# Kernel tuning notes

Hardware: AMD Instinct MI355X
Metric: run time of the kernel (lower is better)

Reference implementation:

```python
import jax, jax.numpy as jnp
import numpy as np

RANK = 8
ALPHA = 16.0
SCALING = ALPHA / RANK


def setup_inputs() -> dict:
    key = jax.random.key(0)
    ks = jax.random.split(key, 13)
    T, B, D = 8, 1024, 1024
    H1, H2, H3 = 2048, 2048, 1024
    r = RANK
    def n(k, shape, scale):
        return jax.random.normal(k, shape, dtype=jnp.float32) * scale
    return {
        "x": n(ks[0], (T, B, D), 1.0),
        "k0": n(ks[1], (D, H1), D ** -0.5),
        "b0": n(ks[2], (H1,), 0.02),
        "d0": n(ks[3], (D, r, T), D ** -0.5),
        "u0": n(ks[4], (r, H1, T), 0.02),  # zeros-init in original; random for nontrivial test
        "k1": n(ks[5], (H1, H2), H1 ** -0.5),
        "b1": n(ks[6], (H2,), 0.02),
        "d1": n(ks[7], (H1, r, T), H1 ** -0.5),
        "u1": n(ks[8], (r, H2, T), 0.02),
        "k2": n(ks[9], (H2, H3), H2 ** -0.5),
        "b2": n(ks[10], (H3,), 0.02),
        "d2": n(ks[11], (H2, r, T), H2 ** -0.5),
        "u2": n(ks[12], (r, H3, T), 0.02),
    }


def _lora_dense(h, k, b, d, u):
    # frozen base matmul: [t,b,i] @ [i,f] -> [t,b,f]
    base = jnp.einsum('tbi,if->tbf', h, k) + b
    # per-task low-rank adapter: down [i,r,t], up [r,f,t]
    delta = jnp.einsum('tbi,irt,rft->tbf', h, d, u) * SCALING
    return base + delta


def reference(x, k0, b0, d0, u0, k1, b1, d1, u1, k2, b2, d2, u2):
    h = jax.nn.relu(_lora_dense(x, k0, b0, d0, u0))
    h = jax.nn.relu(_lora_dense(h, k1, b1, d1, u1))
    h = _lora_dense(h, k2, b2, d2, u2)  # no activation on final layer
    return h
```

## Files before the change

kernel.cpp:

```cpp
#include <hip/hip_runtime.h>

typedef unsigned short u16;
typedef __attribute__((ext_vector_type(8))) __bf16 bf16x8;
typedef __attribute__((ext_vector_type(8))) unsigned short u16x8;
typedef __attribute__((ext_vector_type(4))) float f32x4;

__device__ __forceinline__ float bf2f(u16 h) {
    return __uint_as_float(((unsigned int)h) << 16);
}
__device__ __forceinline__ u16 f2bf(float f) {
    unsigned int u = __float_as_uint(f);
    u += 0x7fffu + ((u >> 16) & 1u);
    return (u16)(u >> 16);
}
__device__ __forceinline__ bf16x8 zero_bf16x8() {
    union { unsigned int u[4]; bf16x8 v; } z;
    z.u[0] = z.u[1] = z.u[2] = z.u[3] = 0u;
    return z.v;
}
__device__ __forceinline__ void gload_lds16(const void* g, void* l) {
    __builtin_amdgcn_global_load_lds(
        (const __attribute__((address_space(1))) unsigned int*)g,
        (__attribute__((address_space(3))) unsigned int*)l, 16, 0, 0);
}
__device__ __forceinline__ void store_out(u16* p, float v)  { *p = f2bf(v); }
__device__ __forceinline__ void store_out(float* p, float v){ *p = v; }


__device__ __forceinline__ void do_cvt(
    const float* __restrict__ in, u16* __restrict__ out, int blk)
{
    int i = (blk * 256 + (int)threadIdx.x) * 8;
    float4 a = *(const float4*)(in + i);
    float4 b = *(const float4*)(in + i + 4);
    u16x8 o;
    o[0] = f2bf(a.x); o[1] = f2bf(a.y); o[2] = f2bf(a.z); o[3] = f2bf(a.w);
    o[4] = f2bf(b.x); o[5] = f2bf(b.y); o[6] = f2bf(b.z); o[7] = f2bf(b.w);
    *(u16x8*)(out + i) = o;
}

__device__ __forceinline__ void do_transpose(
    const float* __restrict__ in, u16* __restrict__ out, int K, int F, int t)
{
    __shared__ u16 tt[32][33];
    int fb = t % (F >> 5), kb = t / (F >> 5);
    int f0 = fb << 5, k0 = kb << 5;
    int lx = threadIdx.x & 31;
    int ly = threadIdx.x >> 5;
#pragma unroll
    for (int i = 0; i < 4; ++i) {
        int k = ly + i * 8;
        tt[k][lx] = f2bf(in[(size_t)(k0 + k) * F + f0 + lx]);
    }
    __syncthreads();
#pragma unroll
    for (int i = 0; i < 4; ++i) {
        int fy = ly + i * 8;
        out[(size_t)(f0 + fy) * K + k0 + lx] = tt[lx][fy];
    }
}

__device__ __forceinline__ void do_prep_d(
    const float* __restrict__ d, u16* __restrict__ o, int K, int blk)
{
    int i = blk * 256 + (int)threadIdx.x;
    int r = i & 7;
    int k = (i >> 3) % K;
    int t = i / (K * 8);
    o[i] = f2bf(d[((size_t)k * 8 + r) * 8 + t]);
}

__device__ __forceinline__ void do_prep_u(
    const float* __restrict__ u, u16* __restrict__ o, int F, int blk)
{
    int i = blk * 256 + (int)threadIdx.x;
    int r = i & 7;
    int f = (i >> 3) % F;
    int t = i / (F * 8);
    o[i] = f2bf(u[((size_t)r * F + f) * 8 + t] * 2.0f);
}

__global__ __launch_bounds__(256) void prep_all(
    const float* x, const float* k0, const float* k1, const float* k2,
    const float* d0, const float* d1, const float* d2,
    const float* u0, const float* u1, const float* u2,
    u16* xb, u16* k0T, u16* k1T, u16* k2T,
    u16* dS0, u16* dS1, u16* dS2, u16* uS0, u16* uS1, u16* uS2)
{
    int b = blockIdx.x;
    if      (b < 4096)  do_cvt(x, xb, b);
    else if (b < 6144)  do_transpose(k0, k0T, 1024, 2048, b - 4096);
    else if (b < 10240) do_transpose(k1, k1T, 2048, 2048, b - 6144);
    else if (b < 12288) do_transpose(k2, k2T, 2048, 1024, b - 10240);
    else if (b < 12544) do_prep_d(d0, dS0, 1024, b - 12288);
    else if (b < 13056) do_prep_d(d1, dS1, 2048, b - 12544);
    else if (b < 13568) do_prep_d(d2, dS2, 2048, b - 13056);
    else if (b < 14080) do_prep_u(u0, uS0, 2048, b - 13568);
    else if (b < 14592) do_prep_u(u1, uS1, 2048, b - 14080);
    else                do_prep_u(u2, uS2, 1024, b - 14592);
}

__global__ __launch_bounds__(256) void lora_down(
    const u16* __restrict__ H, const u16* __restrict__ dS,
    u16* __restrict__ Aout, int K)
{
    int gt   = blockIdx.x * 256 + threadIdx.x;
    int row  = gt >> 3;
    int oct  = gt & 7;
    int task = row >> 10;
    const u16* hrow = H  + (size_t)row * K;
    const u16* dt   = dS + (size_t)task * K * 8;
    float acc[8];
#pragma unroll
    for (int r = 0; r < 8; ++r) acc[r] = 0.f;
    int kpt  = K >> 3;
    int kbeg = oct * kpt;
    for (int kk = kbeg; kk < kbeg + kpt; kk += 8) {
        u16x8 h8 = *(const u16x8*)(hrow + kk);
#pragma unroll
        for (int j = 0; j < 8; ++j) {
            float hv = bf2f(h8[j]);
            u16x8 dv = *(const u16x8*)(dt + (size_t)(kk + j) * 8);
#pragma unroll
            for (int r = 0; r < 8; ++r)
                acc[r] += hv * bf2f(dv[r]);
        }
    }
#pragma unroll
    for (int r = 0; r < 8; ++r) {
        acc[r] += __shfl_xor(acc[r], 1);
        acc[r] += __shfl_xor(acc[r], 2);
        acc[r] += __shfl_xor(acc[r], 4);
    }
    if (oct == 0) {
        u16x8 o;
#pragma unroll
        for (int r = 0; r < 8; ++r) o[r] = f2bf(acc[r]);
        *(u16x8*)(Aout + (size_t)row * 8) = o;
    }
}


#define WVMC do { if constexpr (BN == 256) { \
                    asm volatile("s_waitcnt vmcnt(4)" ::: "memory"); \
                  } else { \
                    asm volatile("s_waitcnt vmcnt(3)" ::: "memory"); } } while (0)
#define WVM0  asm volatile("s_waitcnt vmcnt(0)" ::: "memory")
#define PHASE_END do { __builtin_amdgcn_sched_barrier(0); \
                       __builtin_amdgcn_s_barrier(); } while (0)

#define DS_A(c, mh) do { \
    _Pragma("unroll") for (int mm = 0; mm < 4; ++mm) \
    _Pragma("unroll") for (int ks = 0; ks < 2; ++ks) \
        aF[mm][ks] = *(const bf16x8*)((const char*)&sA[c][0] + \
                       arowb + ((mh)*4+mm)*4096 + (ks ? cb1 : cb0)); } while (0)

#define DS_B(c, nh, bset) do { \
    _Pragma("unroll") for (int nn = 0; nn < NBH; ++nn) \
    _Pragma("unroll") for (int ks = 0; ks < 2; ++ks) \
        bset[nn][ks] = *(const bf16x8*)((const char*)&sB[c][0] + \
                       browb + ((nh)*NBH+nn)*8192 + (ks ? cb1 : cb0)); } while (0)

#define MFMAQ(mh, nh, bset) do { \
    _Pragma("unroll") for (int ks = 0; ks < 2; ++ks) \
    _Pragma("unroll") for (int mm = 0; mm < 4; ++mm) \
    _Pragma("unroll") for (int nn = 0; nn < NBH; ++nn) \
        acc[(mh)*4+mm][(nh)*NBH+nn] = __builtin_amdgcn_mfma_f32_16x16x32_bf16( \
            aF[mm][ks], bset[nn][ks], acc[(mh)*4+mm][(nh)*NBH+nn], 0, 0, 0); } while (0)

#define STAGE_A(c, h, kt) do { \
    _Pragma("unroll") for (int s = 0; s < 2; ++s) \
        gload_lds16((const char*)A + (size_t)(unsigned)(aBase + \
                      ((h)*128 + s*64)*(K*2) + (kt)*128), \
                    (char*)&sA[c][0] + (h)*16384 + s*8192 + tdst); } while (0)

#define STAGE_B(c, h, kt) do { \
    _Pragma("unroll") for (int s = 0; s < SBL; ++s) \
        gload_lds16((const char*)BT + (size_t)(unsigned)(bBase + \
                      ((h)*BNH + s*64)*(K*2) + (kt)*128), \
                    (char*)&sB[c][0] + (h)*(BNH*128) + s*8192 + tdst); } while (0)

template<int RELU, int BN, typename OUT_T>
__global__ __launch_bounds__(512, 2) void gemm_lora8(
    const u16* __restrict__ A, const u16* __restrict__ BT,
    const u16* __restrict__ ALR, const u16* __restrict__ US,
    const float* __restrict__ bias, OUT_T* __restrict__ C,
    int N, int K)
{
    constexpr int SBL = BN / 128;
    constexpr int NBH = BN / 128;
    constexpr int NBN = BN / 64;
    constexpr int BNH = BN / 2;

    __shared__ __align__(16) u16 sA[2][256 * 64];
    __shared__ __align__(16) u16 sB[2][BN * 64];

    const int tid  = threadIdx.x;
    const int lane = tid & 63;
    const int wave = tid >> 6;
    const int wr   = wave >> 2;
    const int wc   = wave & 3;
    const int l15  = lane & 15;
    const int lg   = lane >> 4;

    const int nwg = gridDim.x;
    const int orig = blockIdx.x;
    const int q = nwg >> 3, r = nwg & 7;
    const int x = orig & 7, o = orig >> 3;
    const int wg = (x < r ? x * (q + 1) : r * (q + 1) + (x - r) * q) + o;
    const int nbn  = N / BN;
    const int bm   = wg / nbn;
    const int bn   = wg % nbn;
    const int brow = bm << 8;
    const int bcol = bn * BN;
    const int task = brow >> 10;

    const int trow = tid >> 3;
    const int tkc  = (tid & 7) ^ (trow & 7);
    const int tdst = tid * 16;
    const int aBase = (brow + trow) * (K * 2) + tkc * 16;
    const int bBase = (bcol + trow) * (K * 2) + tkc * 16;

    const int rp    = l15 & 7;
    const int cb0   = ((lg ^ (rp & 3)) << 4) | ((rp & 4) << 4);
    const int cb1   = cb0 ^ 64;
    const int arowb = (wr * 16 + l15) * 128;
    const int browb = (wc * 16 + l15) * 128;

    f32x4 acc[8][NBN];
    const f32x4 zf = {0.f, 0.f, 0.f, 0.f};
#pragma unroll
    for (int m = 0; m < 8; ++m)
#pragma unroll
        for (int n = 0; n < NBN; ++n) acc[m][n] = zf;

    bf16x8 aF[4][2], bF0[NBH][2], bF1[NBH][2];

    STAGE_A(0, 0, 0); STAGE_B(0, 0, 0); STAGE_A(0, 1, 0); STAGE_B(0, 1, 0);
    STAGE_A(1, 0, 1); STAGE_B(1, 0, 1);
    WVMC;
    PHASE_END;

    const int iters = K >> 7;
#pragma unroll 1
    for (int i = 0; i < iters; ++i) {
        const int t1 = 2 * i + 1, t2 = 2 * i + 2, t3 = 2 * i + 3;
        const bool nl = (i + 1 < iters);

        STAGE_A(1, 1, t1);
        DS_A(0, 0); DS_B(0, 0, bF0);
        MFMAQ(0, 0, bF0);
        PHASE_END;
        STAGE_B(1, 1, t1);
        DS_B(0, 1, bF1);
        MFMAQ(0, 1, bF1);
        PHASE_END;
        if (nl) STAGE_A(0, 0, t2);
        DS_A(0, 1);
        MFMAQ(1, 0, bF0);
        PHASE_END;
        if (nl) STAGE_B(0, 0, t2);
        MFMAQ(1, 1, bF1);
        if (nl) { WVMC; } else { WVM0; }
        PHASE_END;
        if (nl) STAGE_A(0, 1, t2);
        DS_A(1, 0); DS_B(1, 0, bF0);
        MFMAQ(0, 0, bF0);
        PHASE_END;
        if (nl) STAGE_B(0, 1, t2);
        DS_B(1, 1, bF1);
        MFMAQ(0, 1, bF1);
        PHASE_END;
        if (nl) STAGE_A(1, 0, t3);
        DS_A(1, 1);
        MFMAQ(1, 0, bF0);
        PHASE_END;
        if (nl) STAGE_B(1, 0, t3);
        MFMAQ(1, 1, bF1);
        if (nl) { WVMC; } else { WVM0; }
        PHASE_END;
    }

    bf16x8 z8 = zero_bf16x8();
    bf16x8 bU[NBN];
#pragma unroll
    for (int n = 0; n < NBN; ++n) {
        int col = bcol + n * 64 + wc * 16 + l15;
        bU[n] = (lg == 0) ? *(const bf16x8*)(US + ((size_t)task * N + col) * 8) : z8;
    }
#pragma unroll
    for (int m = 0; m < 8; ++m) {
        int row = brow + m * 32 + wr * 16 + l15;
        bf16x8 aL = (lg == 0) ? *(const bf16x8*)(ALR + (size_t)row * 8) : z8;
#pragma unroll
        for (int n = 0; n < NBN; ++n)
            acc[m][n] = __builtin_amdgcn_mfma_f32_16x16x32_bf16(
                aL, bU[n], acc[m][n], 0, 0, 0);
    }

#pragma unroll
    for (int n = 0; n < NBN; ++n) {
        int col  = bcol + n * 64 + wc * 16 + l15;
        float bv = bias[col];
#pragma unroll
        for (int m = 0; m < 8; ++m) {
            int row0 = brow + m * 32 + wr * 16 + lg * 4;
#pragma unroll
            for (int rr = 0; rr < 4; ++rr) {
                float v = acc[m][n][rr] + bv;
                if (RELU) v = fmaxf(v, 0.0f);
                store_out(&C[(size_t)(row0 + rr) * N + col], v);
            }
        }
    }
}


extern "C" void kernel_launch(void* const* d_in, const int* in_sizes, int n_in,
                              void* d_out, int out_size, void* d_ws, size_t ws_size,
                              hipStream_t stream) {
    const float* x  = (const float*)d_in[0];
    const float* k0 = (const float*)d_in[1];
    const float* b0 = (const float*)d_in[2];
    const float* d0 = (const float*)d_in[3];
    const float* u0 = (const float*)d_in[4];
    const float* k1 = (const float*)d_in[5];
    const float* b1 = (const float*)d_in[6];
    const float* d1 = (const float*)d_in[7];
    const float* u1 = (const float*)d_in[8];
    const float* k2 = (const float*)d_in[9];
    const float* b2 = (const float*)d_in[10];
    const float* d2 = (const float*)d_in[11];
    const float* u2 = (const float*)d_in[12];

    const int T = 8, B = 1024, D = 1024, H1 = 2048, H2 = 2048, H3 = 1024;
    const int M = T * B;

    u16* w = (u16*)d_ws;
    size_t off = 0;
    u16* xb  = w + off; off += (size_t)M * D;
    u16* k0T = w + off; off += (size_t)H1 * D;
    u16* k1T = w + off; off += (size_t)H2 * H1;
    u16* k2T = w + off; off += (size_t)H3 * H2;
    u16* dS0 = w + off; off += (size_t)T * D * 8;
    u16* dS1 = w + off; off += (size_t)T * H1 * 8;
    u16* dS2 = w + off; off += (size_t)T * H2 * 8;
    u16* uS0 = w + off; off += (size_t)T * H1 * 8;
    u16* uS1 = w + off; off += (size_t)T * H2 * 8;
    u16* uS2 = w + off; off += (size_t)T * H3 * 8;
    u16* h1  = w + off; off += (size_t)M * H1;
    u16* h2  = w + off; off += (size_t)M * H2;
    u16* Ab  = w + off; off += (size_t)M * 8;
    (void)ws_size; (void)in_sizes; (void)n_in; (void)out_size;

    prep_all<<<14848, 256, 0, stream>>>(
        x, k0, k1, k2, d0, d1, d2, u0, u1, u2,
        xb, k0T, k1T, k2T, dS0, dS1, dS2, uS0, uS1, uS2);

    lora_down<<<(M * 8) / 256, 256, 0, stream>>>(xb, dS0, Ab, D);
    gemm_lora8<1, 256, u16><<<(M / 256) * (H1 / 256), 512, 0, stream>>>(
        xb, k0T, Ab, uS0, b0, h1, H1, D);
    lora_down<<<(M * 8) / 256, 256, 0, stream>>>(h1, dS1, Ab, H1);
    gemm_lora8<1, 256, u16><<<(M / 256) * (H2 / 256), 512, 0, stream>>>(
        h1, k1T, Ab, uS1, b1, h2, H2, H1);
    lora_down<<<(M * 8) / 256, 256, 0, stream>>>(h2, dS2, Ab, H2);
    gemm_lora8<0, 128, float><<<(M / 256) * (H3 / 128), 512, 0, stream>>>(
        h2, k2T, Ab, uS2, b2, (float*)d_out, H3, H2);
}
```

Baseline: 261.6 us.

## Software-pipeline LDS fragment loads ahead of MFMAs with double-buffered A registers

Restructures the GEMM main loop so the LDS reads for the next MFMA quadrant are issued one phase early into a second A-fragment register set. This hides LDS latency behind the matrix ops. MFMA blocks are wrapped in s_setprio raises, and vmcnt waits are tightened. The last iteration is peeled, and launch bounds drop to one block per CU. The extra registers lower occupancy, and the tighter wait counts must still match the outstanding loads for correctness.

```diff
diff --git a/kernel.cpp b/kernel.cpp
--- a/kernel.cpp
+++ b/kernel.cpp
@@ -145,28 +145,31 @@
                     asm volatile("s_waitcnt vmcnt(4)" ::: "memory"); \
                   } else { \
                     asm volatile("s_waitcnt vmcnt(3)" ::: "memory"); } } while (0)
+#define VM2   asm volatile("s_waitcnt vmcnt(2)" ::: "memory")
 #define WVM0  asm volatile("s_waitcnt vmcnt(0)" ::: "memory")
 #define PHASE_END do { __builtin_amdgcn_sched_barrier(0); \
                        __builtin_amdgcn_s_barrier(); } while (0)
-
-#define DS_A(c, mh) do { \
+#define PRIO1 __builtin_amdgcn_s_setprio(1)
+#define PRIO0 __builtin_amdgcn_s_setprio(0)
+
+#define DS_A(dst, c, mh) do { \
     _Pragma("unroll") for (int mm = 0; mm < 4; ++mm) \
     _Pragma("unroll") for (int ks = 0; ks < 2; ++ks) \
-        aF[mm][ks] = *(const bf16x8*)((const char*)&sA[c][0] + \
+        dst[mm][ks] = *(const bf16x8*)((const char*)&sA[c][0] + \
                        arowb + ((mh)*4+mm)*4096 + (ks ? cb1 : cb0)); } while (0)
 
-#define DS_B(c, nh, bset) do { \
+#define DS_B(dst, c, nh) do { \
     _Pragma("unroll") for (int nn = 0; nn < NBH; ++nn) \
     _Pragma("unroll") for (int ks = 0; ks < 2; ++ks) \
-        bset[nn][ks] = *(const bf16x8*)((const char*)&sB[c][0] + \
+        dst[nn][ks] = *(const bf16x8*)((const char*)&sB[c][0] + \
                        browb + ((nh)*NBH+nn)*8192 + (ks ? cb1 : cb0)); } while (0)
 
-#define MFMAQ(mh, nh, bset) do { \
+#define MFMAQ(aset, bset, mh, nh) do { \
     _Pragma("unroll") for (int ks = 0; ks < 2; ++ks) \
     _Pragma("unroll") for (int mm = 0; mm < 4; ++mm) \
     _Pragma("unroll") for (int nn = 0; nn < NBH; ++nn) \
         acc[(mh)*4+mm][(nh)*NBH+nn] = __builtin_amdgcn_mfma_f32_16x16x32_bf16( \
-            aF[mm][ks], bset[nn][ks], acc[(mh)*4+mm][(nh)*NBH+nn], 0, 0, 0); } while (0)
+            aset[mm][ks], bset[nn][ks], acc[(mh)*4+mm][(nh)*NBH+nn], 0, 0, 0); } while (0)
 
 #define STAGE_A(c, h, kt) do { \
     _Pragma("unroll") for (int s = 0; s < 2; ++s) \
@@ -181,7 +184,7 @@
                     (char*)&sB[c][0] + (h)*(BNH*128) + s*8192 + tdst); } while (0)
 
 template<int RELU, int BN, typename OUT_T>
-__global__ __launch_bounds__(512, 2) void gemm_lora8(
+__global__ __launch_bounds__(512, 1) void gemm_lora8(
     const u16* __restrict__ A, const u16* __restrict__ BT,
     const u16* __restrict__ ALR, const u16* __restrict__ US,
     const float* __restrict__ bias, OUT_T* __restrict__ C,
@@ -234,51 +237,77 @@
 #pragma unroll
         for (int n = 0; n < NBN; ++n) acc[m][n] = zf;
 
-    bf16x8 aF[4][2], bF0[NBH][2], bF1[NBH][2];
+    bf16x8 aFa[4][2], aFb[4][2], bF0[NBH][2], bF1[NBH][2];
 
     STAGE_A(0, 0, 0); STAGE_B(0, 0, 0); STAGE_A(0, 1, 0); STAGE_B(0, 1, 0);
     STAGE_A(1, 0, 1); STAGE_B(1, 0, 1);
     WVMC;
     PHASE_END;
+    DS_A(aFa, 0, 0); DS_B(bF0, 0, 0);
 
     const int iters = K >> 7;
 #pragma unroll 1
-    for (int i = 0; i < iters; ++i) {
+    for (int i = 0; i < iters - 1; ++i) {
         const int t1 = 2 * i + 1, t2 = 2 * i + 2, t3 = 2 * i + 3;
-        const bool nl = (i + 1 < iters);
-
+        DS_B(bF1, 0, 1);
         STAGE_A(1, 1, t1);
-        DS_A(0, 0); DS_B(0, 0, bF0);
-        MFMAQ(0, 0, bF0);
-        PHASE_END;
+        PRIO1; MFMAQ(aFa, bF0, 0, 0); PRIO0;
+        PHASE_END;
+        DS_A(aFb, 0, 1);
         STAGE_B(1, 1, t1);
-        DS_B(0, 1, bF1);
-        MFMAQ(0, 1, bF1);
-        PHASE_END;
-        if (nl) STAGE_A(0, 0, t2);
-        DS_A(0, 1);
-        MFMAQ(1, 0, bF0);
-        PHASE_END;
-        if (nl) STAGE_B(0, 0, t2);
-        MFMAQ(1, 1, bF1);
-        if (nl) { WVMC; } else { WVM0; }
-        PHASE_END;
-        if (nl) STAGE_A(0, 1, t2);
-        DS_A(1, 0); DS_B(1, 0, bF0);
-        MFMAQ(0, 0, bF0);
-        PHASE_END;
-        if (nl) STAGE_B(0, 1, t2);
-        DS_B(1, 1, bF1);
-        MFMAQ(0, 1, bF1);
-        PHASE_END;
-        if (nl) STAGE_A(1, 0, t3);
-        DS_A(1, 1);
-        MFMAQ(1, 0, bF0);
-        PHASE_END;
-        if (nl) STAGE_B(1, 0, t3);
-        MFMAQ(1, 1, bF1);
-        if (nl) { WVMC; } else { WVM0; }
-        PHASE_END;
+        PRIO1; MFMAQ(aFa, bF1, 0, 1); PRIO0;
+        PHASE_END;
+        STAGE_A(0, 0, t2);
+        PRIO1; MFMAQ(aFb, bF0, 1, 0); PRIO0;
+        VM2;
+        PHASE_END;
+        DS_A(aFa, 1, 0); DS_B(bF0, 1, 0);
+        STAGE_B(0, 0, t2);
+        PRIO1; MFMAQ(aFb, bF1, 1, 1); PRIO0;
+        PHASE_END;
+        DS_B(bF1, 1, 1);
+        STAGE_A(0, 1, t2);
+        PRIO1; MFMAQ(aFa, bF0, 0, 0); PRIO0;
+        PHASE_END;
+        DS_A(aFb, 1, 1);
+        STAGE_B(0, 1, t2);
+        PRIO1; MFMAQ(aFa, bF1, 0, 1); PRIO0;
+        PHASE_END;
+        STAGE_A(1, 0, t3);
+        PRIO1; MFMAQ(aFb, bF0, 1, 0); PRIO0;
+        VM2;
+        PHASE_END;
+        DS_A(aFa, 0, 0); DS_B(bF0, 0, 0);
+        STAGE_B(1, 0, t3);
+        PRIO1; MFMAQ(aFb, bF1, 1, 1); PRIO0;
+        PHASE_END;
+    }
+
+    {
+        const int t1 = 2 * iters - 1;
+        DS_B(bF1, 0, 1);
+        STAGE_A(1, 1, t1);
+        PRIO1; MFMAQ(aFa, bF0, 0, 0); PRIO0;
+        PHASE_END;
+        DS_A(aFb, 0, 1);
+        STAGE_B(1, 1, t1);
+        PRIO1; MFMAQ(aFa, bF1, 0, 1); PRIO0;
+        PHASE_END;
+        PRIO1; MFMAQ(aFb, bF0, 1, 0); PRIO0;
+        WVM0;
+        PHASE_END;
+        DS_A(aFa, 1, 0); DS_B(bF0, 1, 0);
+        PRIO1; MFMAQ(aFb, bF1, 1, 1); PRIO0;
+        PHASE_END;
+        DS_B(bF1, 1, 1);
+        PRIO1; MFMAQ(aFa, bF0, 0, 0); PRIO0;
+        PHASE_END;
+        DS_A(aFb, 1, 1);
+        PRIO1; MFMAQ(aFa, bF1, 0, 1); PRIO0;
+        PHASE_END;
+        PRIO1; MFMAQ(aFb, bF0, 1, 0); PRIO0;
+        PHASE_END;
+        PRIO1; MFMAQ(aFb, bF1, 1, 1); PRIO0;
     }
 
     bf16x8 z8 = zero_bf16x8();
```

Result: slower. 361.5 us (+38.2%).
